# Optimization experiments

Hardware: AMD Instinct MI355X
Metric: run time of the kernel (lower is better)

## Reference

```python
import jax, jax.numpy as jnp
import numpy as np

MAX_ITERS = 20
TOL = 1e-6
STEP = 1.0
EPS = 1e-7
CLIP = 1e-7


def _normalize(x, axis=-1):
    n = jnp.linalg.norm(x, axis=axis, keepdims=True)
    return x / jnp.maximum(n, 1e-12)


def _safe_acos(x):
    return jnp.arccos(jnp.clip(x, -1.0 + CLIP, 1.0 - CLIP))


def setup_inputs() -> dict:
    key = jax.random.key(0)
    NC, K, N, D = 1000, 8, 32, 128
    X_groups = jax.random.normal(key, (NC, K, N, D), dtype=jnp.float32)
    return {"X_groups": X_groups}


def reference(X_groups):
    # X_groups: (NC, K, N, D)
    NC, K, N, D = X_groups.shape
    X = X_groups.reshape(NC * K, N, D)
    Xn = _normalize(X)                      # (G, N, D) unit vectors
    mu = _normalize(jnp.mean(Xn, axis=1))   # (G, D) init mean

    done = jnp.array(False)
    for _ in range(MAX_ITERS):
        dots = jnp.einsum('gd,gnd->gn', mu, Xn)             # (G, N)
        theta = _safe_acos(dots)
        sin_t = jnp.maximum(jnp.sin(theta), EPS)
        diff = Xn - dots[..., None] * mu[:, None, :]        # (G, N, D)
        log_vecs = (theta / sin_t)[..., None] * diff        # log map
        v = jnp.mean(log_vecs, axis=1)                      # (G, D)
        v_norm = jnp.maximum(jnp.linalg.norm(v, axis=-1, keepdims=True), EPS)
        done = done | (jnp.max(v_norm) < TOL)               # global convergence (as in torch .item() check)
        v_step = STEP * v
        vs_norm = jnp.maximum(jnp.linalg.norm(v_step, axis=-1, keepdims=True), EPS)
        mu_new = jnp.cos(vs_norm) * mu + jnp.sin(vs_norm) * (v_step / vs_norm)  # exp map
        mu_new = _normalize(mu_new)
        mu = jnp.where(done, mu, mu_new)

    # calc_cluster_distance: features (G, N, D) @ means (G, D)
    sims = jnp.einsum('gnd,gd->gn', Xn, mu)
    sims = jnp.clip(sims, -1 + CLIP, 1 - CLIP)
    loss = jnp.mean(jnp.sum(jnp.arccos(sims) ** 2, axis=-1))
    return loss
```

## Files before the change

kernel.cpp:

```cpp
#include <hip/hip_runtime.h>
#include <stdint.h>

#define MAX_ITERS 20
#define EPSV 1e-7f
#define CLIPV 1e-7f
#define PI_F 3.14159265358979f
#define PIO2_F 1.57079632679490f

typedef __attribute__((ext_vector_type(8))) short short8;
typedef __attribute__((ext_vector_type(4))) float f4;

__device__ __forceinline__ f4 mfma_bf16(short8 a, short8 b, f4 c) {
    return __builtin_amdgcn_mfma_f32_16x16x32_bf16(a, b, c, 0, 0, 0);
}

__device__ __forceinline__ float rl(float v, int l) {
    return __int_as_float(__builtin_amdgcn_readlane(__float_as_int(v), l));
}

template <int CTRL>
__device__ __forceinline__ float dpp_add(float v) {
    int p = __builtin_amdgcn_update_dpp(0, __float_as_int(v), CTRL, 0xF, 0xF, true);
    return v + __int_as_float(p);
}

__device__ __forceinline__ float rowsum32(float v) {
    v = dpp_add<0xB1>(v);
    v = dpp_add<0x4E>(v);
    v = dpp_add<0x141>(v);
    v = dpp_add<0x140>(v);
    return rl(v, 0) + rl(v, 16);
}

__device__ __forceinline__ float fast_acos(float x) {
    float a = fabsf(x);
    bool big = a > 0.5f;
    float z = big ? 0.5f * (1.0f - a) : x * x;
    float s = big ? sqrtf(z) : x;
    float p = fmaf(z, fmaf(z, fmaf(z, fmaf(z, 4.2163199048e-2f, 2.4181311049e-2f),
                                   4.5470025998e-2f), 7.4953002686e-2f),
                   1.6666752422e-1f);
    float r = fmaf(s * z, p, s);
    float big_val = (x < 0.0f) ? (PI_F - 2.0f * r) : (2.0f * r);
    return big ? big_val : (PIO2_F - r);
}

__device__ __forceinline__ void cvt_hilo(const float* v, short8& hi, short8& lo) {
#pragma unroll
    for (int i = 0; i < 8; ++i) {
        float x = v[i];
        uint32_t u = __float_as_uint(x);
        float hf = __uint_as_float(u & 0xFFFF0000u);
        float lf = x - hf;
        hi[i] = (short)(u >> 16);
        lo[i] = (short)(__float_as_uint(lf) >> 16);
    }
}

__global__ void __launch_bounds__(128) karcher(const float* __restrict__ X,
                                               float* __restrict__ ws,
                                               int n_groups) {
    __shared__ float sG[2][32 * 33];

    const int lane = threadIdx.x & 63;
    const int wid  = threadIdx.x >> 6;
    const int g    = blockIdx.x * 2 + wid;

    const float* Xg = X + (size_t)g * (32 * 128);
    const int col  = lane & 15;
    const int quad = lane >> 4;

    f4 acc00 = {0.f, 0.f, 0.f, 0.f};
    f4 acc01 = acc00, acc10 = acc00, acc11 = acc00;
#pragma unroll
    for (int kc = 0; kc < 4; ++kc) {
        const float* p0 = Xg + col * 128 + kc * 32 + quad * 8;
        const float* p1 = p0 + 16 * 128;
        float r0[8], r1[8];
        *(float4*)(r0)     = *(const float4*)(p0);
        *(float4*)(r0 + 4) = *(const float4*)(p0 + 4);
        *(float4*)(r1)     = *(const float4*)(p1);
        *(float4*)(r1 + 4) = *(const float4*)(p1 + 4);
        short8 H0, L0, H1, L1;
        cvt_hilo(r0, H0, L0);
        cvt_hilo(r1, H1, L1);
        acc00 = mfma_bf16(H0, H0, acc00);
        acc00 = mfma_bf16(H0, L0, acc00);
        acc00 = mfma_bf16(L0, H0, acc00);
        acc01 = mfma_bf16(H0, H1, acc01);
        acc01 = mfma_bf16(H0, L1, acc01);
        acc01 = mfma_bf16(L0, H1, acc01);
        acc10 = mfma_bf16(H1, H0, acc10);
        acc10 = mfma_bf16(H1, L0, acc10);
        acc10 = mfma_bf16(L1, H0, acc10);
        acc11 = mfma_bf16(H1, H1, acc11);
        acc11 = mfma_bf16(H1, L1, acc11);
        acc11 = mfma_bf16(L1, H1, acc11);
    }

    float* Gw = sG[wid];
#pragma unroll
    for (int i = 0; i < 4; ++i) {
        int rw = quad * 4 + i;
        Gw[rw * 33 + col]             = acc00[i];
        Gw[rw * 33 + col + 16]        = acc01[i];
        Gw[(rw + 16) * 33 + col]      = acc10[i];
        Gw[(rw + 16) * 33 + col + 16] = acc11[i];
    }
    __syncthreads();

    const int r = lane & 31;
    float Grow[32];
#pragma unroll
    for (int j = 0; j < 32; ++j) Grow[j] = Gw[r * 33 + j];
    const float inv_  = 1.0f / fmaxf(sqrtf(Gw[r * 33 + r]), 1e-12f);
    const float inv32 = inv_ * (1.0f / 32.0f);

    float a = inv32;
    float ga;
    {
        float s0 = 0, s1 = 0, s2 = 0, s3 = 0;
#pragma unroll
        for (int j = 0; j < 8; ++j) {
            s0 = fmaf(Grow[j],      rl(a, j),      s0);
            s1 = fmaf(Grow[j + 8],  rl(a, j + 8),  s1);
            s2 = fmaf(Grow[j + 16], rl(a, j + 16), s2);
            s3 = fmaf(Grow[j + 24], rl(a, j + 24), s3);
        }
        ga = (s0 + s1) + (s2 + s3);
        float n2   = rowsum32(a * ga);
        float inv0 = 1.0f / fmaxf(sqrtf(n2), 1e-12f);
        a  *= inv0;
        ga *= inv0;
    }

    for (int it = 0; it < MAX_ITERS; ++it) {
        float dotr = ga * inv_;
        float x  = fminf(fmaxf(dotr, -1.0f + CLIPV), 1.0f - CLIPV);
        float th = fast_acos(x);
        float st = fmaxf(sqrtf(fmaxf(1.0f - x * x, 0.0f)), EPSV);
        float w  = __fdividef(th, st);
        float u  = w * inv32;
        float s0 = 0, s1 = 0, s2 = 0, s3 = 0;
#pragma unroll
        for (int j = 0; j < 8; ++j) {
            s0 = fmaf(Grow[j],      rl(u, j),      s0);
            s1 = fmaf(Grow[j + 8],  rl(u, j + 8),  s1);
            s2 = fmaf(Grow[j + 16], rl(u, j + 16), s2);
            s3 = fmaf(Grow[j + 24], rl(u, j + 24), s3);
        }
        float gu  = (s0 + s1) + (s2 + s3);
        float C   = rowsum32(w * dotr);
        float c32 = C * (1.0f / 32.0f);
        float beta = u  - c32 * a;
        float gb   = gu - c32 * ga;
        float vv = rowsum32(beta * gb);
        float vs = fmaxf(sqrtf(fmaxf(vv, 0.0f)), EPSV);
        float cv = __cosf(vs);
        float sv = __fdividef(__sinf(vs), vs);
        a  = fmaf(sv, beta, cv * a);
        ga = fmaf(sv, gb, cv * ga);
        if (vs < 1e-6f) break;
    }

    float xf = fminf(fmaxf(ga * inv_, -1.0f + CLIPV), 1.0f - CLIPV);
    float t  = fast_acos(xf);
    float ls = rowsum32(t * t);
    if (lane == 0) ws[blockIdx.x * 2 + wid] = ls;
}

__global__ void __launch_bounds__(256) reduce_partials(const float* __restrict__ ws,
                                                       float* __restrict__ out,
                                                       int n, float scale) {
    __shared__ float sred[4];
    float s = 0.f;
    for (int i = threadIdx.x; i < n; i += 256) s += ws[i];
#pragma unroll
    for (int m = 32; m >= 1; m >>= 1) s += __shfl_xor(s, m, 64);
    const int lane = threadIdx.x & 63, wid = threadIdx.x >> 6;
    if (lane == 0) sred[wid] = s;
    __syncthreads();
    if (threadIdx.x == 0)
        out[0] = ((sred[0] + sred[1]) + (sred[2] + sred[3])) * scale;
}

extern "C" void kernel_launch(void* const* d_in, const int* in_sizes, int n_in,
                              void* d_out, int out_size, void* d_ws, size_t ws_size,
                              hipStream_t stream) {
    const float* X = (const float*)d_in[0];
    float* out = (float*)d_out;
    float* ws = (float*)d_ws;
    int n_groups = in_sizes[0] / (32 * 128);
    int blocks = n_groups / 2;
    karcher<<<blocks, 128, 0, stream>>>(X, ws, n_groups);
    reduce_partials<<<1, 256, 0, stream>>>(ws, out, n_groups, 1.0f / (float)n_groups);
}
```

Baseline: 229.3 us.

## Pack two groups per wavefront and use LDS matvec instead of readlanes

Each 64-lane wavefront now handles two groups, one per 32-lane half, instead of leaving half the lanes doing redundant work. The Gram matvec reads the per-iteration vector from LDS with float4 loads instead of 32 scalar readlanes. Reductions switch to DPP plus ds_swizzle so each half gets its own sum. The C computation is simplified algebraically, and the block grows to 256 threads (8 groups) with a wave-wide early-exit vote. The trade-off is more LDS traffic, and a converged half keeps iterating until the other half also converges.

Measured after the change: 215.9 us. 1.06x faster.

```diff
diff --git a/kernel.cpp b/kernel.cpp
--- a/kernel.cpp
+++ b/kernel.cpp
@@ -6,16 +6,13 @@
 #define CLIPV 1e-7f
 #define PI_F 3.14159265358979f
 #define PIO2_F 1.57079632679490f
+#define SGS 36
 
 typedef __attribute__((ext_vector_type(8))) short short8;
 typedef __attribute__((ext_vector_type(4))) float f4;
 
 __device__ __forceinline__ f4 mfma_bf16(short8 a, short8 b, f4 c) {
     return __builtin_amdgcn_mfma_f32_16x16x32_bf16(a, b, c, 0, 0, 0);
-}
-
-__device__ __forceinline__ float rl(float v, int l) {
-    return __int_as_float(__builtin_amdgcn_readlane(__float_as_int(v), l));
 }
 
 template <int CTRL>
@@ -24,12 +21,14 @@
     return v + __int_as_float(p);
 }
 
-__device__ __forceinline__ float rowsum32(float v) {
+__device__ __forceinline__ float halfsum32(float v) {
     v = dpp_add<0xB1>(v);
     v = dpp_add<0x4E>(v);
     v = dpp_add<0x141>(v);
     v = dpp_add<0x140>(v);
-    return rl(v, 0) + rl(v, 16);
+    v += __int_as_float(
+        __builtin_amdgcn_ds_swizzle(__float_as_int(v), 0x401F));
+    return v;
 }
 
 __device__ __forceinline__ float fast_acos(float x) {
@@ -57,78 +56,94 @@
     }
 }
 
-__global__ void __launch_bounds__(128) karcher(const float* __restrict__ X,
-                                               float* __restrict__ ws,
-                                               int n_groups) {
-    __shared__ float sG[2][32 * 33];
+__global__ void __launch_bounds__(256, 4) karcher(const float* __restrict__ X,
+                                                  float* __restrict__ ws) {
+    __shared__ float sG[8][32 * SGS];
+    __shared__ float sU[8][32];
 
     const int lane = threadIdx.x & 63;
     const int wid  = threadIdx.x >> 6;
-    const int g    = blockIdx.x * 2 + wid;
-
-    const float* Xg = X + (size_t)g * (32 * 128);
+    const int half = lane >> 5;
+    const int r    = lane & 31;
+    const int slot = wid * 2;
+    const int g0   = blockIdx.x * 8 + wid * 2;
+
     const int col  = lane & 15;
     const int quad = lane >> 4;
 
-    f4 acc00 = {0.f, 0.f, 0.f, 0.f};
-    f4 acc01 = acc00, acc10 = acc00, acc11 = acc00;
-#pragma unroll
-    for (int kc = 0; kc < 4; ++kc) {
-        const float* p0 = Xg + col * 128 + kc * 32 + quad * 8;
-        const float* p1 = p0 + 16 * 128;
-        float r0[8], r1[8];
-        *(float4*)(r0)     = *(const float4*)(p0);
-        *(float4*)(r0 + 4) = *(const float4*)(p0 + 4);
-        *(float4*)(r1)     = *(const float4*)(p1);
-        *(float4*)(r1 + 4) = *(const float4*)(p1 + 4);
-        short8 H0, L0, H1, L1;
-        cvt_hilo(r0, H0, L0);
-        cvt_hilo(r1, H1, L1);
-        acc00 = mfma_bf16(H0, H0, acc00);
-        acc00 = mfma_bf16(H0, L0, acc00);
-        acc00 = mfma_bf16(L0, H0, acc00);
-        acc01 = mfma_bf16(H0, H1, acc01);
-        acc01 = mfma_bf16(H0, L1, acc01);
-        acc01 = mfma_bf16(L0, H1, acc01);
-        acc10 = mfma_bf16(H1, H0, acc10);
-        acc10 = mfma_bf16(H1, L0, acc10);
-        acc10 = mfma_bf16(L1, H0, acc10);
-        acc11 = mfma_bf16(H1, H1, acc11);
-        acc11 = mfma_bf16(H1, L1, acc11);
-        acc11 = mfma_bf16(L1, H1, acc11);
-    }
-
-    float* Gw = sG[wid];
-#pragma unroll
-    for (int i = 0; i < 4; ++i) {
-        int rw = quad * 4 + i;
-        Gw[rw * 33 + col]             = acc00[i];
-        Gw[rw * 33 + col + 16]        = acc01[i];
-        Gw[(rw + 16) * 33 + col]      = acc10[i];
-        Gw[(rw + 16) * 33 + col + 16] = acc11[i];
-    }
-    __syncthreads();
-
-    const int r = lane & 31;
+#pragma unroll
+    for (int h = 0; h < 2; ++h) {
+        const float* Xg = X + (size_t)(g0 + h) * (32 * 128);
+        f4 acc00 = {0.f, 0.f, 0.f, 0.f};
+        f4 acc01 = acc00, acc10 = acc00, acc11 = acc00;
+#pragma unroll
+        for (int kc = 0; kc < 4; ++kc) {
+            const float* p0 = Xg + col * 128 + kc * 32 + quad * 8;
+            const float* p1 = p0 + 16 * 128;
+            float r0[8], r1[8];
+            *(float4*)(r0)     = *(const float4*)(p0);
+            *(float4*)(r0 + 4) = *(const float4*)(p0 + 4);
+            *(float4*)(r1)     = *(const float4*)(p1);
+            *(float4*)(r1 + 4) = *(const float4*)(p1 + 4);
+            short8 H0, L0, H1, L1;
+            cvt_hilo(r0, H0, L0);
+            cvt_hilo(r1, H1, L1);
+            acc00 = mfma_bf16(H0, H0, acc00);
+            acc00 = mfma_bf16(H0, L0, acc00);
+            acc00 = mfma_bf16(L0, H0, acc00);
+            acc01 = mfma_bf16(H0, H1, acc01);
+            acc01 = mfma_bf16(H0, L1, acc01);
+            acc01 = mfma_bf16(L0, H1, acc01);
+            acc10 = mfma_bf16(H1, H0, acc10);
+            acc10 = mfma_bf16(H1, L0, acc10);
+            acc10 = mfma_bf16(L1, H0, acc10);
+            acc11 = mfma_bf16(H1, H1, acc11);
+            acc11 = mfma_bf16(H1, L1, acc11);
+            acc11 = mfma_bf16(L1, H1, acc11);
+        }
+        float* Gh = sG[slot + h];
+#pragma unroll
+        for (int i = 0; i < 4; ++i) {
+            int rw = quad * 4 + i;
+            Gh[rw * SGS + col]             = acc00[i];
+            Gh[rw * SGS + col + 16]        = acc01[i];
+            Gh[(rw + 16) * SGS + col]      = acc10[i];
+            Gh[(rw + 16) * SGS + col + 16] = acc11[i];
+        }
+    }
+
+    float* Gw = sG[slot + half];
     float Grow[32];
 #pragma unroll
-    for (int j = 0; j < 32; ++j) Grow[j] = Gw[r * 33 + j];
-    const float inv_  = 1.0f / fmaxf(sqrtf(Gw[r * 33 + r]), 1e-12f);
+    for (int c = 0; c < 8; ++c)
+        *(float4*)(&Grow[c * 4]) = *(const float4*)(&Gw[r * SGS + c * 4]);
+    const float inv_  = 1.0f / fmaxf(sqrtf(Gw[r * SGS + r]), 1e-12f);
     const float inv32 = inv_ * (1.0f / 32.0f);
+
+    float* sUrow = sU[slot + half];
+    const float4* ub = (const float4*)sUrow;
+
+#define MATVEC(uval, guout)                                                  \
+    {                                                                        \
+        sUrow[r] = (uval);                                                   \
+        float m0 = 0, m1 = 0, m2 = 0, m3 = 0;                                \
+        _Pragma("unroll") for (int c = 0; c < 8; ++c) {                      \
+            float4 uc = ub[c];                                               \
+            float* mp = (c & 1) ? ((c & 2) ? &m3 : &m1)                      \
+                                : ((c & 2) ? &m2 : &m0);                     \
+            *mp = fmaf(Grow[4 * c + 3], uc.w,                                \
+                  fmaf(Grow[4 * c + 2], uc.z,                                \
+                  fmaf(Grow[4 * c + 1], uc.y,                                \
+                  fmaf(Grow[4 * c + 0], uc.x, *mp))));                       \
+        }                                                                    \
+        (guout) = (m0 + m1) + (m2 + m3);                                     \
+    }
 
     float a = inv32;
     float ga;
+    MATVEC(a, ga);
     {
-        float s0 = 0, s1 = 0, s2 = 0, s3 = 0;
-#pragma unroll
-        for (int j = 0; j < 8; ++j) {
-            s0 = fmaf(Grow[j],      rl(a, j),      s0);
-            s1 = fmaf(Grow[j + 8],  rl(a, j + 8),  s1);
-            s2 = fmaf(Grow[j + 16], rl(a, j + 16), s2);
-            s3 = fmaf(Grow[j + 24], rl(a, j + 24), s3);
-        }
-        ga = (s0 + s1) + (s2 + s3);
-        float n2   = rowsum32(a * ga);
+        float n2   = halfsum32(a * ga);
         float inv0 = 1.0f / fmaxf(sqrtf(n2), 1e-12f);
         a  *= inv0;
         ga *= inv0;
@@ -141,32 +156,25 @@
         float st = fmaxf(sqrtf(fmaxf(1.0f - x * x, 0.0f)), EPSV);
         float w  = __fdividef(th, st);
         float u  = w * inv32;
-        float s0 = 0, s1 = 0, s2 = 0, s3 = 0;
-#pragma unroll
-        for (int j = 0; j < 8; ++j) {
-            s0 = fmaf(Grow[j],      rl(u, j),      s0);
-            s1 = fmaf(Grow[j + 8],  rl(u, j + 8),  s1);
-            s2 = fmaf(Grow[j + 16], rl(u, j + 16), s2);
-            s3 = fmaf(Grow[j + 24], rl(u, j + 24), s3);
-        }
-        float gu  = (s0 + s1) + (s2 + s3);
-        float C   = rowsum32(w * dotr);
-        float c32 = C * (1.0f / 32.0f);
-        float beta = u  - c32 * a;
-        float gb   = gu - c32 * ga;
-        float vv = rowsum32(beta * gb);
+        float gu;
+        MATVEC(u, gu);
+        float c    = halfsum32(u * ga);
+        float beta = u  - c * a;
+        float gb   = gu - c * ga;
+        float vv = halfsum32(beta * gb);
         float vs = fmaxf(sqrtf(fmaxf(vv, 0.0f)), EPSV);
         float cv = __cosf(vs);
         float sv = __fdividef(__sinf(vs), vs);
         a  = fmaf(sv, beta, cv * a);
         ga = fmaf(sv, gb, cv * ga);
-        if (vs < 1e-6f) break;
+        if (__all(vs < 1e-6f)) break;
     }
 
     float xf = fminf(fmaxf(ga * inv_, -1.0f + CLIPV), 1.0f - CLIPV);
     float t  = fast_acos(xf);
-    float ls = rowsum32(t * t);
-    if (lane == 0) ws[blockIdx.x * 2 + wid] = ls;
+    float ls = halfsum32(t * t);
+    if (r == 0) ws[g0 + half] = ls;
+#undef MATVEC
 }
 
 __global__ void __launch_bounds__(256) reduce_partials(const float* __restrict__ ws,
@@ -191,7 +199,7 @@
     float* out = (float*)d_out;
     float* ws = (float*)d_ws;
     int n_groups = in_sizes[0] / (32 * 128);
-    int blocks = n_groups / 2;
-    karcher<<<blocks, 128, 0, stream>>>(X, ws, n_groups);
+    int blocks = n_groups / 8;
+    karcher<<<blocks, 256, 0, stream>>>(X, ws);
     reduce_partials<<<1, 256, 0, stream>>>(ws, out, n_groups, 1.0f / (float)n_groups);
 }
```
